# Kernel tuning notes

Hardware: AMD Instinct MI355X
Metric: run time of the kernel (lower is better)

The kernel has to match this reference:

```python
import jax, jax.numpy as jnp
import numpy as np

N, K, D, C, H = 200000, 256, 12, 9, 32
EPS = 1e-8


def setup_inputs() -> dict:
    key = jax.random.key(0)
    ks = jax.random.split(key, 8)
    probe_pos = jax.random.uniform(ks[0], (N, 3), dtype=jnp.float32)
    mu = jax.random.uniform(ks[1], (K, 3), dtype=jnp.float32)
    log_s = jax.random.normal(ks[2], (K, 3), dtype=jnp.float32) * 0.3 - 1.5
    # quaternions near identity (w~1) as in the torch init
    q = jax.random.normal(ks[3], (K, 4), dtype=jnp.float32) * 0.1 + jnp.array([1.0, 0.0, 0.0, 0.0], jnp.float32)
    F = jax.random.normal(ks[4], (K, D), dtype=jnp.float32) * 0.1
    W1 = jax.random.normal(ks[5], (D + 3, H), dtype=jnp.float32) / np.sqrt(D + 3).astype(np.float32)
    b1 = jnp.zeros((H,), jnp.float32)
    W2 = jax.random.normal(ks[6], (H, C), dtype=jnp.float32) / np.sqrt(H).astype(np.float32)
    b2 = jnp.zeros((C,), jnp.float32)
    return {"probe_pos": probe_pos, "mu": mu, "log_s": log_s, "q": q,
            "F": F, "W1": W1, "b1": b1, "W2": W2, "b2": b2}


def quaternion_to_rotation_matrix(q):
    # q: [K,4] (w,x,y,z) -> [K,3,3]
    q = q / (jnp.linalg.norm(q, axis=-1, keepdims=True) + EPS)
    w, x, y, z = q[..., 0], q[..., 1], q[..., 2], q[..., 3]
    r0 = jnp.stack([1 - 2 * y * y - 2 * z * z, 2 * x * y - 2 * w * z, 2 * x * z + 2 * w * y], axis=-1)
    r1 = jnp.stack([2 * x * y + 2 * w * z, 1 - 2 * x * x - 2 * z * z, 2 * y * z - 2 * w * x], axis=-1)
    r2 = jnp.stack([2 * x * z - 2 * w * y, 2 * y * z + 2 * w * x, 1 - 2 * x * x - 2 * y * y], axis=-1)
    return jnp.stack([r0, r1, r2], axis=-2)


def reference(probe_pos, mu, log_s, q, F, W1, b1, W2, b2):
    s = jnp.exp(log_s)                                   # [K,3]
    R = quaternion_to_rotation_matrix(q)                 # [K,3,3]
    s_inv_sq = 1.0 / (s ** 2 + EPS)                      # [K,3]
    # precision = R @ diag(s_inv_sq) @ R^T -> [K,3,3]
    precision = jnp.einsum('kij,kj,klj->kil', R, s_inv_sq, R)
    diff = probe_pos[:, None, :] - mu[None, :, :]        # [N,K,3]
    mahal = jnp.einsum('nki,kij,nkj->nk', diff, precision, diff)  # [N,K]
    gvals = jnp.exp(-0.5 * mahal)                        # [N,K]
    radii = 3.0 * s.max(axis=1)                          # [K]
    dist = jnp.linalg.norm(diff, axis=2)                 # [N,K]
    gvals = gvals * (dist < radii[None, :]).astype(gvals.dtype)
    weights = gvals / (gvals.sum(axis=1, keepdims=True) + EPS)    # [N,K]
    latent = weights @ F                                 # [N,D]
    mlp_in = jnp.concatenate([latent, probe_pos], axis=1)         # [N,D+3]
    h = jax.nn.relu(mlp_in @ W1 + b1)                    # [N,H]
    sh = h @ W2 + b2                                     # [N,C]
    return (sh, latent, weights)
```

## Files before the change

### kernel.cpp

```cpp
#include <hip/hip_runtime.h>

#define KG 256
#define DD 12
#define HH 32
#define CC 9
#define TPB 256

__global__ __launch_bounds__(256) void gp_pre(
    const float* __restrict__ mu, const float* __restrict__ log_s,
    const float* __restrict__ q, const float* __restrict__ F,
    float* __restrict__ Ct) {
  int k = threadIdx.x;
  if (k >= KG) return;
  float qw = q[k*4+0], qx = q[k*4+1], qy = q[k*4+2], qz = q[k*4+3];
  float nrm = sqrtf(qw*qw + qx*qx + qy*qy + qz*qz);
  float isn = 1.0f / (nrm + 1e-8f);
  qw *= isn; qx *= isn; qy *= isn; qz *= isn;
  float R00 = 1.f - 2.f*(qy*qy + qz*qz);
  float R01 = 2.f*(qx*qy - qw*qz);
  float R02 = 2.f*(qx*qz + qw*qy);
  float R10 = 2.f*(qx*qy + qw*qz);
  float R11 = 1.f - 2.f*(qx*qx + qz*qz);
  float R12 = 2.f*(qy*qz - qw*qx);
  float R20 = 2.f*(qx*qz - qw*qy);
  float R21 = 2.f*(qy*qz + qw*qx);
  float R22 = 1.f - 2.f*(qx*qx + qy*qy);
  float s0 = expf(log_s[k*3+0]);
  float s1 = expf(log_s[k*3+1]);
  float s2 = expf(log_s[k*3+2]);
  float si0 = 1.f/(s0*s0 + 1e-8f);
  float si1 = 1.f/(s1*s1 + 1e-8f);
  float si2 = 1.f/(s2*s2 + 1e-8f);
  float P00 = R00*si0*R00 + R01*si1*R01 + R02*si2*R02;
  float P01 = R00*si0*R10 + R01*si1*R11 + R02*si2*R12;
  float P02 = R00*si0*R20 + R01*si1*R21 + R02*si2*R22;
  float P11 = R10*si0*R10 + R11*si1*R11 + R12*si2*R12;
  float P12 = R10*si0*R20 + R11*si1*R21 + R12*si2*R22;
  float P22 = R20*si0*R20 + R21*si1*R21 + R22*si2*R22;
  float m0 = mu[k*3+0], m1 = mu[k*3+1], m2 = mu[k*3+2];
  float b0 = P00*m0 + P01*m1 + P02*m2;
  float b1v = P01*m0 + P11*m1 + P12*m2;
  float b2v = P02*m0 + P12*m1 + P22*m2;
  float cterm = m0*b0 + m1*b1v + m2*b2v;
  const float f = -0.7213475204444817f;
  float* c = Ct + k*32;
  c[0] = f*P00;  c[1] = f*P11;  c[2] = f*P22;
  c[3] = 2.f*f*P01;  c[4] = 2.f*f*P02;  c[5] = 2.f*f*P12;
  c[6] = -2.f*f*b0;  c[7] = -2.f*f*b1v; c[8] = -2.f*f*b2v;
  c[9] = f*cterm;
  c[10] = -2.f*m0;  c[11] = -2.f*m1;  c[12] = -2.f*m2;
  c[13] = m0*m0 + m1*m1 + m2*m2;
  float smax = fmaxf(s0, fmaxf(s1, s2));
  c[14] = (3.f*smax)*(3.f*smax);
  c[15] = 0.f;
  #pragma unroll
  for (int d = 0; d < DD; ++d) c[16+d] = F[k*DD + d];
  c[28] = c[29] = c[30] = c[31] = 0.f;
}

__device__ __forceinline__ float gauss_eval(
    const float* __restrict__ c,
    float xx, float yy, float zz, float xy, float xz, float yz,
    float x, float y, float z, float pp) {
  float tp = fmaf(c[0], xx, c[9]);
  tp = fmaf(c[1], yy, tp);
  tp = fmaf(c[2], zz, tp);
  tp = fmaf(c[3], xy, tp);
  tp = fmaf(c[4], xz, tp);
  tp = fmaf(c[5], yz, tp);
  tp = fmaf(c[6], x, tp);
  tp = fmaf(c[7], y, tp);
  tp = fmaf(c[8], z, tp);
  float d2 = pp + c[13];
  d2 = fmaf(c[10], x, d2);
  d2 = fmaf(c[11], y, d2);
  d2 = fmaf(c[12], z, d2);
  float e = __builtin_amdgcn_exp2f(tp);
  return (d2 < c[14]) ? e : 0.0f;
}

__global__ __launch_bounds__(TPB, 4) void gp_main(
    const float* __restrict__ pos, const float* __restrict__ Ct,
    const float* __restrict__ W1, const float* __restrict__ b1,
    const float* __restrict__ W2, const float* __restrict__ b2,
    float* __restrict__ sh_out, float* __restrict__ lat_out,
    float* __restrict__ w_out, int N) {
  __shared__ float pxyzi[TPB][4];
  const int tid = threadIdx.x;
  const int pbase = blockIdx.x * TPB;
  const int p = pbase + tid;
  const bool valid = (p < N);
  const int pc = valid ? p : (N - 1);
  const float x = pos[pc*3+0], y = pos[pc*3+1], z = pos[pc*3+2];
  const float xx = x*x, yy = y*y, zz = z*z;
  const float xy = x*y, xz = x*z, yz = y*z;
  const float pp = xx + yy + zz;

  float lat[DD];
  #pragma unroll
  for (int j = 0; j < DD; ++j) lat[j] = 0.0f;
  float denom = 1e-8f;
  #pragma unroll 4
  for (int k = 0; k < KG; ++k) {
    const float* c = Ct + (k << 5);
    float g = gauss_eval(c, xx, yy, zz, xy, xz, yz, x, y, z, pp);
    denom += g;
    #pragma unroll
    for (int j = 0; j < DD; ++j) lat[j] = fmaf(g, c[16+j], lat[j]);
  }
  const float inv = 1.0f / denom;

  *(float4*)pxyzi[tid] = make_float4(x, y, z, inv);

  float lf[DD];
  #pragma unroll
  for (int j = 0; j < DD; ++j) lf[j] = lat[j] * inv;
  if (valid) {
    float4* lo = (float4*)(lat_out + (size_t)p * DD);
    lo[0] = make_float4(lf[0], lf[1], lf[2],  lf[3]);
    lo[1] = make_float4(lf[4], lf[5], lf[6],  lf[7]);
    lo[2] = make_float4(lf[8], lf[9], lf[10], lf[11]);
  }

  {
    float h[HH];
    #pragma unroll
    for (int j = 0; j < HH; ++j) h[j] = b1[j];
    #pragma unroll
    for (int i = 0; i < DD; ++i) {
      const float v = lf[i];
      #pragma unroll
      for (int j = 0; j < HH; ++j) h[j] = fmaf(v, W1[i*HH + j], h[j]);
    }
    #pragma unroll
    for (int j = 0; j < HH; ++j) h[j] = fmaf(x, W1[12*HH + j], h[j]);
    #pragma unroll
    for (int j = 0; j < HH; ++j) h[j] = fmaf(y, W1[13*HH + j], h[j]);
    #pragma unroll
    for (int j = 0; j < HH; ++j) h[j] = fmaf(z, W1[14*HH + j], h[j]);
    float o[CC];
    #pragma unroll
    for (int c2 = 0; c2 < CC; ++c2) o[c2] = b2[c2];
    #pragma unroll
    for (int j = 0; j < HH; ++j) {
      const float a = fmaxf(h[j], 0.0f);
      #pragma unroll
      for (int c2 = 0; c2 < CC; ++c2) o[c2] = fmaf(a, W2[j*CC + c2], o[c2]);
    }
    if (valid) {
      float* so = sh_out + (size_t)p * CC;
      #pragma unroll
      for (int c2 = 0; c2 < CC; ++c2) so[c2] = o[c2];
    }
  }

  const int lane = tid & 63;
  const int wbase = tid & ~63;
  float cb[4][16];
  #pragma unroll
  for (int u = 0; u < 4; ++u) {
    const float4* r = (const float4*)(Ct + (((lane << 2) + u) << 5));
    *(float4*)&cb[u][0]  = r[0];
    *(float4*)&cb[u][4]  = r[1];
    *(float4*)&cb[u][8]  = r[2];
    *(float4*)&cb[u][12] = r[3];
  }
  __syncthreads();

  #pragma unroll 2
  for (int pi = 0; pi < 64; ++pi) {
    const int lp = wbase + pi;
    const float4 b = *(const float4*)pxyzi[lp];
    const float bx = b.x, by = b.y, bz = b.z, binv = b.w;
    const float bxx = bx*bx, byy = by*by, bzz = bz*bz;
    const float bxy = bx*by, bxz = bx*bz, byz = by*bz;
    const float bpp = bxx + byy + bzz;
    float wv[4];
    #pragma unroll
    for (int u = 0; u < 4; ++u)
      wv[u] = gauss_eval(cb[u], bxx, byy, bzz, bxy, bxz, byz,
                         bx, by, bz, bpp) * binv;
    const int gp2 = pbase + lp;
    if (gp2 < N)
      *(float4*)&w_out[(size_t)gp2 * KG + (lane << 2)] =
          make_float4(wv[0], wv[1], wv[2], wv[3]);
  }
}

extern "C" void kernel_launch(void* const* d_in, const int* in_sizes, int n_in,
                              void* d_out, int out_size, void* d_ws, size_t ws_size,
                              hipStream_t stream) {
  const float* probe_pos = (const float*)d_in[0];
  const float* mu        = (const float*)d_in[1];
  const float* log_s     = (const float*)d_in[2];
  const float* q         = (const float*)d_in[3];
  const float* F         = (const float*)d_in[4];
  const float* W1        = (const float*)d_in[5];
  const float* b1        = (const float*)d_in[6];
  const float* W2        = (const float*)d_in[7];
  const float* b2        = (const float*)d_in[8];
  const int N = in_sizes[0] / 3;

  float* Ct = (float*)d_ws;
  float* sh_out  = (float*)d_out;
  float* lat_out = sh_out + (size_t)N*CC;
  float* w_out   = lat_out + (size_t)N*DD;

  gp_pre<<<1, 256, 0, stream>>>(mu, log_s, q, F, Ct);
  const int nb = (N + TPB - 1) / TPB;
  gp_main<<<nb, TPB, 0, stream>>>(probe_pos, Ct, W1, b1, W2, b2,
                                  sh_out, lat_out, w_out, N);
}
```

Before: 315.0 us.

## Split Gaussian reduction across four waves per 64-point block

Each block now handles 64 points instead of 256, and each of the four waves reduces over a 64-Gaussian slice of K. Partial latents and denominators go to shared memory and are summed there. The MLP runs on only one wave per block, and the weight write-out now has each thread own one Gaussian and write scalars. This shortens the per-thread serial K loop and raises occupancy, at the cost of extra LDS traffic, barriers, and an MLP phase that leaves three waves idle.

```diff
diff --git a/kernel.cpp b/kernel.cpp
--- a/kernel.cpp
+++ b/kernel.cpp
@@ -5,6 +5,10 @@
 #define HH 32
 #define CC 9
 #define TPB 256
+#define PPB 64
+#define KSPL 4
+#define KPT 64
+#define PSTR 16
 
 __global__ __launch_bounds__(256) void gp_pre(
     const float* __restrict__ mu, const float* __restrict__ log_s,
@@ -79,111 +83,123 @@
   return (d2 < c[14]) ? e : 0.0f;
 }
 
-__global__ __launch_bounds__(TPB, 4) void gp_main(
+__global__ __launch_bounds__(TPB, 6) void gp_main(
     const float* __restrict__ pos, const float* __restrict__ Ct,
     const float* __restrict__ W1, const float* __restrict__ b1,
     const float* __restrict__ W2, const float* __restrict__ b2,
     float* __restrict__ sh_out, float* __restrict__ lat_out,
     float* __restrict__ w_out, int N) {
-  __shared__ float pxyzi[TPB][4];
-  const int tid = threadIdx.x;
-  const int pbase = blockIdx.x * TPB;
-  const int p = pbase + tid;
-  const bool valid = (p < N);
-  const int pc = valid ? p : (N - 1);
-  const float x = pos[pc*3+0], y = pos[pc*3+1], z = pos[pc*3+2];
+  __shared__ float part[KSPL * PPB * PSTR];
+  __shared__ float4 pxyzi[PPB];
+  const int tid  = threadIdx.x;
+  const int lane = tid & 63;
+  const int wv   = tid >> 6;
+  const int pbase = blockIdx.x * PPB;
+
+  if (tid < PPB) {
+    int p = pbase + tid; if (p >= N) p = N - 1;
+    pxyzi[tid] = make_float4(pos[p*3+0], pos[p*3+1], pos[p*3+2], 0.f);
+  }
+  __syncthreads();
+
+  const float4 pv = pxyzi[lane];
+  const float x = pv.x, y = pv.y, z = pv.z;
   const float xx = x*x, yy = y*y, zz = z*z;
   const float xy = x*y, xz = x*z, yz = y*z;
   const float pp = xx + yy + zz;
 
+  const int kg = __builtin_amdgcn_readfirstlane(wv);
+  const float* cbase = Ct + (size_t)(kg * KPT) * 32;
   float lat[DD];
   #pragma unroll
   for (int j = 0; j < DD; ++j) lat[j] = 0.0f;
-  float denom = 1e-8f;
+  float dsum = 0.0f;
   #pragma unroll 4
-  for (int k = 0; k < KG; ++k) {
-    const float* c = Ct + (k << 5);
+  for (int i = 0; i < KPT; ++i) {
+    const float* c = cbase + (i << 5);
     float g = gauss_eval(c, xx, yy, zz, xy, xz, yz, x, y, z, pp);
-    denom += g;
+    dsum += g;
     #pragma unroll
     for (int j = 0; j < DD; ++j) lat[j] = fmaf(g, c[16+j], lat[j]);
   }
-  const float inv = 1.0f / denom;
-
-  *(float4*)pxyzi[tid] = make_float4(x, y, z, inv);
-
-  float lf[DD];
+  {
+    float* pw = part + (wv * PPB + lane) * PSTR;
+    *(float4*)(pw + 0) = make_float4(lat[0], lat[1], lat[2],  lat[3]);
+    *(float4*)(pw + 4) = make_float4(lat[4], lat[5], lat[6],  lat[7]);
+    *(float4*)(pw + 8) = make_float4(lat[8], lat[9], lat[10], lat[11]);
+    *(float4*)(pw +12) = make_float4(dsum, 0.f, 0.f, 0.f);
+  }
+
+  float cb[16];
+  {
+    const float4* r = (const float4*)(Ct + ((size_t)tid << 5));
+    *(float4*)&cb[0]  = r[0];
+    *(float4*)&cb[4]  = r[1];
+    *(float4*)&cb[8]  = r[2];
+    *(float4*)&cb[12] = r[3];
+  }
+  __syncthreads();
+
   #pragma unroll
-  for (int j = 0; j < DD; ++j) lf[j] = lat[j] * inv;
-  if (valid) {
-    float4* lo = (float4*)(lat_out + (size_t)p * DD);
-    lo[0] = make_float4(lf[0], lf[1], lf[2],  lf[3]);
-    lo[1] = make_float4(lf[4], lf[5], lf[6],  lf[7]);
-    lo[2] = make_float4(lf[8], lf[9], lf[10], lf[11]);
-  }
-
-  {
-    float h[HH];
-    #pragma unroll
-    for (int j = 0; j < HH; ++j) h[j] = b1[j];
-    #pragma unroll
-    for (int i = 0; i < DD; ++i) {
-      const float v = lf[i];
+  for (int s = tid; s < PPB*13; s += TPB) {
+    const int pr = s / 13, j = s - pr*13;
+    float a = part[(0*PPB + pr)*PSTR + j] + part[(1*PPB + pr)*PSTR + j]
+            + part[(2*PPB + pr)*PSTR + j] + part[(3*PPB + pr)*PSTR + j];
+    part[pr*PSTR + j] = a;
+  }
+  __syncthreads();
+
+  float inv = 0.0f;
+  if (tid < PPB) {
+    inv = 1.0f / (part[tid*PSTR + 12] + 1e-8f);
+    pxyzi[tid].w = inv;
+  }
+  __syncthreads();
+
+  if (tid < PPB*3) {
+    const int pr = tid / 3, q = tid - pr*3;
+    if (pbase + pr < N) {
+      const float iv = pxyzi[pr].w;
+      const float* r = part + pr*PSTR + q*4;
+      *(float4*)(lat_out + (size_t)pbase*DD + tid*4) =
+          make_float4(r[0]*iv, r[1]*iv, r[2]*iv, r[3]*iv);
+    }
+  }
+
+  if (tid < PPB && pbase + tid < N) {
+    float in15[15];
+    #pragma unroll
+    for (int j = 0; j < DD; ++j) in15[j] = part[tid*PSTR + j] * inv;
+    in15[12] = x; in15[13] = y; in15[14] = z;
+    float o[CC];
+    #pragma unroll
+    for (int c2 = 0; c2 < CC; ++c2) o[c2] = b2[c2];
+    #pragma unroll 2
+    for (int j = 0; j < HH; ++j) {
+      float a = b1[j];
       #pragma unroll
-      for (int j = 0; j < HH; ++j) h[j] = fmaf(v, W1[i*HH + j], h[j]);
-    }
-    #pragma unroll
-    for (int j = 0; j < HH; ++j) h[j] = fmaf(x, W1[12*HH + j], h[j]);
-    #pragma unroll
-    for (int j = 0; j < HH; ++j) h[j] = fmaf(y, W1[13*HH + j], h[j]);
-    #pragma unroll
-    for (int j = 0; j < HH; ++j) h[j] = fmaf(z, W1[14*HH + j], h[j]);
-    float o[CC];
-    #pragma unroll
-    for (int c2 = 0; c2 < CC; ++c2) o[c2] = b2[c2];
-    #pragma unroll
-    for (int j = 0; j < HH; ++j) {
-      const float a = fmaxf(h[j], 0.0f);
+      for (int i = 0; i < 15; ++i) a = fmaf(in15[i], W1[i*HH + j], a);
+      a = fmaxf(a, 0.f);
       #pragma unroll
       for (int c2 = 0; c2 < CC; ++c2) o[c2] = fmaf(a, W2[j*CC + c2], o[c2]);
     }
-    if (valid) {
-      float* so = sh_out + (size_t)p * CC;
-      #pragma unroll
-      for (int c2 = 0; c2 < CC; ++c2) so[c2] = o[c2];
-    }
-  }
-
-  const int lane = tid & 63;
-  const int wbase = tid & ~63;
-  float cb[4][16];
-  #pragma unroll
-  for (int u = 0; u < 4; ++u) {
-    const float4* r = (const float4*)(Ct + (((lane << 2) + u) << 5));
-    *(float4*)&cb[u][0]  = r[0];
-    *(float4*)&cb[u][4]  = r[1];
-    *(float4*)&cb[u][8]  = r[2];
-    *(float4*)&cb[u][12] = r[3];
-  }
-  __syncthreads();
-
-  #pragma unroll 2
-  for (int pi = 0; pi < 64; ++pi) {
-    const int lp = wbase + pi;
-    const float4 b = *(const float4*)pxyzi[lp];
+    float* so = sh_out + (size_t)(pbase + tid) * CC;
+    #pragma unroll
+    for (int c2 = 0; c2 < CC; ++c2) so[c2] = o[c2];
+  }
+
+  #pragma unroll 4
+  for (int pi = 0; pi < PPB; ++pi) {
+    const int lp = (pi + (wv << 4)) & (PPB - 1);
+    const float4 b = pxyzi[lp];
     const float bx = b.x, by = b.y, bz = b.z, binv = b.w;
     const float bxx = bx*bx, byy = by*by, bzz = bz*bz;
     const float bxy = bx*by, bxz = bx*bz, byz = by*bz;
     const float bpp = bxx + byy + bzz;
-    float wv[4];
-    #pragma unroll
-    for (int u = 0; u < 4; ++u)
-      wv[u] = gauss_eval(cb[u], bxx, byy, bzz, bxy, bxz, byz,
-                         bx, by, bz, bpp) * binv;
+    const float wval = gauss_eval(cb, bxx, byy, bzz, bxy, bxz, byz,
+                                  bx, by, bz, bpp) * binv;
     const int gp2 = pbase + lp;
-    if (gp2 < N)
-      *(float4*)&w_out[(size_t)gp2 * KG + (lane << 2)] =
-          make_float4(wv[0], wv[1], wv[2], wv[3]);
+    if (gp2 < N) w_out[(size_t)gp2 * KG + tid] = wval;
   }
 }
 
@@ -207,7 +223,7 @@
   float* w_out   = lat_out + (size_t)N*DD;
 
   gp_pre<<<1, 256, 0, stream>>>(mu, log_s, q, F, Ct);
-  const int nb = (N + TPB - 1) / TPB;
+  const int nb = (N + PPB - 1) / PPB;
   gp_main<<<nb, TPB, 0, stream>>>(probe_pos, Ct, W1, b1, W2, b2,
                                   sh_out, lat_out, w_out, N);
 }
```

Result: faster. 289.1 us (median of 2 runs) (-8.2%).
